# Performance work log

Measured on AMD Instinct MI355X. Metric: run time of the kernel, lower is better.

Reference implementation:

```python
import jax, jax.numpy as jnp
import numpy as np

TEMPERATURE = 0.07
BASE_TEMPERATURE = 0.07


def setup_inputs() -> dict:
    key = jax.random.key(0)
    k1, k2, k3, k4 = jax.random.split(key, 4)
    b, N, d = 1024, 32768, 128
    output_q = jax.random.normal(k1, (b, d), dtype=jnp.float32)
    output_q = output_q / jnp.linalg.norm(output_q, axis=1, keepdims=True)
    queue_all = jax.random.normal(k2, (b + N, d), dtype=jnp.float32)
    queue_all = queue_all / jnp.linalg.norm(queue_all, axis=1, keepdims=True)
    # class flags in [-1, 20); -1 means 'invalid / ignore' per the module's special-casing
    flags = jax.random.randint(k3, (b, 1), -1, 20, dtype=jnp.int32)
    queue_flags_all = jax.random.randint(k4, (b + N, 1), -1, 20, dtype=jnp.int32)
    return {
        "output_q": output_q,
        "queue_all": queue_all,
        "flags": flags,
        "queue_flags_all": queue_flags_all,
        "n_iter": 100,
    }


def reference(output_q, queue_all, flags, queue_flags_all, n_iter):
    b = output_q.shape[0]
    queue = queue_all[b:]            # [N, d]
    qflags = queue_flags_all[b:]     # [N, 1]
    # anchor-vs-queue logits, max-subtracted for stability (max is detached)
    logits = (output_q @ queue.T) / TEMPERATURE                       # [b, N]
    logits = logits - jax.lax.stop_gradient(jnp.max(logits, axis=1, keepdims=True))
    # positive mask: same flag; rows with flag == -1 are fully zeroed
    row_m1 = flags[:, 0] == -1                                        # [b]
    mask_pos = (flags == qflags.T) & (~row_m1[:, None])               # [b, N]
    logits = jnp.where(row_m1[:, None], 0.0, logits)
    lfp = logits * mask_pos                                           # logits_filtered_pos
    if n_iter >= 0:
        # per-row flag revision: if far more entries below the row mean than above,
        # the row's pseudo-label is deemed wrong -> flag := 0, positives zeroed
        mean_sim = lfp.mean(axis=1, keepdims=True)                    # [b, 1]
        pos_cnt = jnp.sum(lfp >= mean_sim, axis=1).astype(jnp.float32)
        wrong_cnt = jnp.sum(lfp < mean_sim, axis=1).astype(jnp.float32)
        revise = (wrong_cnt / (pos_cnt + 1e-6)) > 10.0                # [b]
        flags = jnp.where(revise[:, None], 0, flags)
        lfp = jnp.where(revise[:, None], 0.0, lfp)
    # zero out queue columns whose flag is -1
    col_m1 = qflags[:, 0] == -1                                       # [N]
    logits = jnp.where(col_m1[None, :], 0.0, logits)
    exp_logits = jnp.exp(logits)
    # exact-zero logits (masked entries AND the natural row max) give exp == 1 -> drop them
    exp_logits = exp_logits * (exp_logits != 1.0)
    row_sum = exp_logits.sum(axis=1, keepdims=True)                   # [b, 1]
    log_prob = lfp - jnp.log(row_sum + 1e-12)                         # [b, N]
    num_nonzero = jnp.sum(lfp != 0.0).astype(jnp.float32)             # global count (scalar)
    row_lp = log_prob.sum(axis=1)                                     # [b]
    cond = (num_nonzero > 0) & (row_sum[:, 0] > 0) & (row_lp < 0)     # per-row gate
    loss = jnp.sum(jnp.where(cond, row_lp / num_nonzero, 0.0)) / b
    loss = -(TEMPERATURE / BASE_TEMPERATURE) * loss
    return loss.reshape(1), flags
```

## Files before the change

### kernel.cpp

```cpp
#include <hip/hip_runtime.h>
#include <stdint.h>


typedef short bf16x8 __attribute__((ext_vector_type(8)));
typedef unsigned short ushort8v __attribute__((ext_vector_type(8)));
typedef float f32x4 __attribute__((ext_vector_type(4)));

#define INV_T 14.285714285714286f
#define K2E 20.609929155698604f

__device__ __forceinline__ unsigned short f2bf(float x) {
    unsigned u = __float_as_uint(x);
    return (unsigned short)((u + 0x7FFFu + ((u >> 16) & 1u)) >> 16);
}
__device__ __forceinline__ ushort8v cvt8(const float4* s4) {
    float4 a = s4[0], b = s4[1];
    ushort8v v;
    v[0] = f2bf(a.x); v[1] = f2bf(a.y); v[2] = f2bf(a.z); v[3] = f2bf(a.w);
    v[4] = f2bf(b.x); v[5] = f2bf(b.y); v[6] = f2bf(b.z); v[7] = f2bf(b.w);
    return v;
}
__device__ __forceinline__ void gload_lds16(const void* g, void* l) {
    __builtin_amdgcn_global_load_lds(
        (const __attribute__((address_space(1))) unsigned int*)g,
        (__attribute__((address_space(3))) unsigned int*)l, 16, 0, 0);
}

__global__ void convert_kernel(const float* __restrict__ Q,
                               const float* __restrict__ Kv,
                               const int* __restrict__ qf,
                               unsigned short* __restrict__ Qb,
                               char* __restrict__ KbB,
                               unsigned* __restrict__ histP,
                               unsigned* __restrict__ wrongA, int N, int b) {
    __shared__ unsigned lh[32];
    const int t = threadIdx.x;
    const int blk = blockIdx.x;
    if (blk < 64) {
        if (t < 32) lh[t] = 0u;
        __syncthreads();
        int j0 = blk * 512;
        atomicAdd(&lh[qf[j0 + t] + 1], 1u);
        atomicAdd(&lh[qf[j0 + 256 + t] + 1], 1u);
        __syncthreads();
        if (t < 32) histP[blk * 32 + t] = lh[t];
    }
    int i = blk * 256 + t;
    if (i < b) wrongA[i] = 0u;
    int nk = N * 16;
    if (i < nk) {
        int row = i >> 4, kc = i & 15;
        ushort8v v = cvt8(reinterpret_cast<const float4*>(
            Kv + (size_t)row * 128 + kc * 8));
        int tb = row >> 6, rr = row & 63;
        int off = tb * 16384 + ((rr * 256 + kc * 16) ^ ((rr & 7) << 4));
        *reinterpret_cast<ushort8v*>(KbB + off) = v;
    } else if (i < nk + b * 16) {
        int j = i - nk;
        int row = j >> 4, kc = j & 15;
        ushort8v v = cvt8(reinterpret_cast<const float4*>(
            Q + (size_t)row * 128 + kc * 8));
        *reinterpret_cast<ushort8v*>((char*)Qb + row * 256 + kc * 16) = v;
    }
}

__global__ __launch_bounds__(512, 2) void gemm_kernel(
    const unsigned short* __restrict__ Qb, const char* __restrict__ KbB,
    const int* __restrict__ flags, const int* __restrict__ qf,
    float4* __restrict__ part, int b)
{
    __shared__ __align__(16) char sB[2][16384];
    const int tid = threadIdx.x;
    const int lane = tid & 63, g = lane >> 4, q = lane & 15;
    const int wave = tid >> 6, wr = wave >> 1, wc = wave & 1;
    const int bx = blockIdx.x;
    const int r0 = blockIdx.y * 128;

    bf16x8 af[2][4];
#pragma unroll
    for (int mi = 0; mi < 2; ++mi) {
        int row = r0 + 32 * wr + 16 * mi + q;
#pragma unroll
        for (int ks = 0; ks < 4; ++ks)
            af[mi][ks] = *reinterpret_cast<const bf16x8*>(
                Qb + (size_t)row * 128 + ks * 32 + g * 8);
    }
    unsigned flpack[2];
#pragma unroll
    for (int mi = 0; mi < 2; ++mi) {
        unsigned p = 0;
#pragma unroll
        for (int reg = 0; reg < 4; ++reg) {
            int f = flags[r0 + 32 * wr + 16 * mi + 4 * g + reg];
            unsigned byte = (f < 0) ? 255u : (unsigned)(f + 1);
            p |= byte << (8 * reg);
        }
        flpack[mi] = p;
    }

    float bestp[8], se[8], sl[8];
#pragma unroll
    for (int r = 0; r < 8; ++r) { bestp[r] = -3.0e38f; se[r] = 0.f; sl[r] = 0.f; }

#define STAGE(buf, gt)                                                 \
    {                                                                  \
        const char* s_ = KbB + (size_t)(gt) * 16384 + tid * 16;        \
        char* d_ = &sB[buf][tid * 16];                                 \
        gload_lds16(s_, d_);                                           \
        gload_lds16(s_ + 8192, d_ + 8192);                             \
    }

    STAGE(0, bx * 8);

    for (int t = 0; t < 8; ++t) {
        __syncthreads();
        if (t < 7) STAGE((t + 1) & 1, bx * 8 + t + 1);
        const char* bb = sB[t & 1];

        f32x4 acc[2][2];
#pragma unroll
        for (int mi = 0; mi < 2; ++mi)
#pragma unroll
            for (int ni = 0; ni < 2; ++ni) acc[mi][ni] = (f32x4){0, 0, 0, 0};

#pragma unroll
        for (int ks = 0; ks < 4; ++ks) {
            bf16x8 bf[2];
#pragma unroll
            for (int ni = 0; ni < 2; ++ni) {
                int rr = 32 * wc + 16 * ni + q;
                bf[ni] = *reinterpret_cast<const bf16x8*>(
                    bb + ((rr * 256 + ks * 64 + g * 16) ^ ((rr & 7) << 4)));
            }
#pragma unroll
            for (int mi = 0; mi < 2; ++mi)
#pragma unroll
                for (int ni = 0; ni < 2; ++ni)
                    acc[mi][ni] = __builtin_amdgcn_mfma_f32_16x16x32_bf16(
                        af[mi][ks], bf[ni], acc[mi][ni], 0, 0, 0);
        }

        int cb = bx * 512 + t * 64 + 32 * wc + q;
        unsigned qv1[2] = {(unsigned)(qf[cb] + 1), (unsigned)(qf[cb + 16] + 1)};
#pragma unroll
        for (int mi = 0; mi < 2; ++mi)
#pragma unroll
            for (int reg = 0; reg < 4; ++reg) {
                int rr8 = mi * 4 + reg;
                unsigned fc = (flpack[mi] >> (8 * reg)) & 255u;
                float bp = bestp[rr8], s = se[rr8], l = sl[rr8];
#pragma unroll
                for (int ni = 0; ni < 2; ++ni) {
                    float dot = acc[mi][ni][reg];
                    float e = exp2f(dot * K2E);
                    s += (qv1[ni] == 0u) ? 0.f : e;
                    l += (qv1[ni] == fc) ? dot : 0.f;
                    float dp = __uint_as_float(
                        (__float_as_uint(dot) & ~31u) | qv1[ni]);
                    bp = fmaxf(bp, dp);
                }
                bestp[rr8] = bp; se[rr8] = s; sl[rr8] = l;
            }
    }

    float4* scr = (float4*)sB;
#pragma unroll
    for (int rr8 = 0; rr8 < 8; ++rr8) {
        float bp = bestp[rr8], s = se[rr8], l = sl[rr8];
#pragma unroll
        for (int off = 1; off < 16; off <<= 1) {
            float ob = __shfl_xor(bp, off);
            float os = __shfl_xor(s, off);
            float ol = __shfl_xor(l, off);
            bp = fmaxf(bp, ob);
            s += os;
            l += ol;
        }
        if (q == 0) {
            int rl = 32 * wr + 16 * (rr8 >> 2) + 4 * g + (rr8 & 3);
            scr[wc * 128 + rl] = make_float4(bp, s, l, 0.f);
        }
    }
    __syncthreads();
    if (tid < 128) {
        float4 a = scr[tid], c = scr[128 + tid];
        part[(size_t)bx * b + r0 + tid] =
            make_float4(fmaxf(a.x, c.x), a.y + c.y, a.z + c.z, 0.f);
    }
}

__global__ __launch_bounds__(256) void reduce_kernel(
    const float4* __restrict__ part, const int* __restrict__ flags,
    const unsigned* __restrict__ histP, float* __restrict__ bestA,
    int* __restrict__ flagsA, float* __restrict__ sumlA,
    float* __restrict__ sumexpA, unsigned* __restrict__ cntA, int b)
{
    __shared__ float4 red[4][64];
    __shared__ unsigned sh[32];
    const int t = threadIdx.x;
    if (t < 32) {
        unsigned s = 0;
#pragma unroll
        for (int i = 0; i < 64; ++i) s += histP[i * 32 + t];
        sh[t] = s;
    }
    const int rl = t & 63;
    const int r = blockIdx.x * 64 + rl;
    const int pg = t >> 6;
    float bp = -3.0e38f, s = 0.f, l = 0.f;
    for (int cs = pg; cs < 64; cs += 4) {
        float4 p = part[(size_t)cs * b + r];
        bp = fmaxf(bp, p.x);
        s += p.y;
        l += p.z;
    }
    red[pg][rl] = make_float4(bp, s, l, 0.f);
    __syncthreads();
    if (t < 64) {
        const int rr = blockIdx.x * 64 + t;
        bp = -3.0e38f; s = 0.f; l = 0.f;
#pragma unroll
        for (int i = 0; i < 4; ++i) {
            float4 p = red[i][t];
            bp = fmaxf(bp, p.x);
            s += p.y;
            l += p.z;
        }
        bestA[rr] = bp;
        flagsA[rr] = (int)(__float_as_uint(bp) & 31u);
        sumexpA[rr] = s;
        sumlA[rr] = l;
        int f = flags[rr];
        cntA[rr] = (f >= 0) ? sh[f + 1] : 0u;
    }
}

__global__ void fallback_kernel(const float* __restrict__ Q,
                                const float* __restrict__ Kv,
                                const int* __restrict__ flags,
                                const int* __restrict__ qf,
                                const float* __restrict__ bestA,
                                const float* __restrict__ sumlA,
                                const unsigned* __restrict__ cntA,
                                unsigned* __restrict__ wrongA, int N)
{
    const int r = blockIdx.x;
    unsigned c = cntA[r];
    float ub = (float)c / ((float)(N - (int)c) + 1e-6f);
    if (!(ub > 10.0f)) return;

    __shared__ float sQ[128];
    const int tid = threadIdx.x;
    if (tid < 128) sQ[tid] = Q[(size_t)r * 128 + tid];
    __syncthreads();

    float m = bestA[r] * INV_T;
    float mean = (INV_T * sumlA[r] - (float)c * m) / (float)N;
    int f = flags[r];
    int wp = 0;
    for (int j = tid; j < N; j += 256) {
        float dot = 0.f;
        const float* kr = Kv + (size_t)j * 128;
        for (int k = 0; k < 128; ++k) dot += sQ[k] * kr[k];
        bool mask = (f == qf[j]) && (f != -1);
        float lfp = mask ? (dot * INV_T - m) : 0.f;
        if (lfp < mean) wp++;
    }
    atomicAdd(&wrongA[r], (unsigned)wp);
}

__global__ void final_kernel(const int* __restrict__ flags,
                             const int* __restrict__ n_iter_p,
                             const float* __restrict__ bestA,
                             const int* __restrict__ flagsA,
                             const float* __restrict__ sumlA,
                             const float* __restrict__ sumexpA,
                             const unsigned* __restrict__ cntA,
                             const unsigned* __restrict__ wrongA,
                             float* __restrict__ out, int N, int b)
{
    __shared__ float redf[1024];
    __shared__ unsigned redu[1024];
    const int r = threadIdx.x;

    int f = flags[r];
    bool row_m1 = (f == -1);
    float mdot = bestA[r];
    float m = mdot * INV_T;
    int qmax1 = flagsA[r];
    float s = sumexpA[r];
    float l = sumlA[r];
    unsigned cnt = cntA[r];

    float rowsum;
    if (row_m1) {
        rowsum = 0.f;
    } else {
        float adj = s - ((qmax1 == 0) ? 0.f : exp2f(mdot * K2E));
        rowsum = exp2f(-mdot * K2E) * adj;
        rowsum = fmaxf(rowsum, 0.f);
    }
    float sum_lfp = INV_T * l - (float)cnt * m;
    bool ispos = (!row_m1) && (qmax1 - 1 == f);
    unsigned nnz = cnt - (ispos ? 1u : 0u);

    int nit = *n_iter_p;
    bool revise = false;
    if (nit >= 0) {
        float ub = (float)cnt / ((float)(N - (int)cnt) + 1e-6f);
        if (ub > 10.0f) {
            unsigned wr = wrongA[r];
            float wf = (float)wr;
            float pf = (float)(N - (int)wr);
            revise = (wf / (pf + 1e-6f)) > 10.0f;
        }
    }
    out[1 + r] = (float)(revise ? 0 : f);
    float eff_suml = revise ? 0.f : sum_lfp;
    unsigned eff_nnz = revise ? 0u : nnz;

    redu[r] = eff_nnz;
    __syncthreads();
    for (int ss = 512; ss > 0; ss >>= 1) {
        if (r < ss) redu[r] += redu[r + ss];
        __syncthreads();
    }
    unsigned total_nnz = redu[0];
    __syncthreads();

    float row_lp = eff_suml - (float)N * logf(rowsum + 1e-12f);
    float contrib = (total_nnz > 0u && rowsum > 0.f && row_lp < 0.f)
                        ? row_lp / (float)total_nnz
                        : 0.f;
    redf[r] = contrib;
    __syncthreads();
    for (int ss = 512; ss > 0; ss >>= 1) {
        if (r < ss) redf[r] += redf[r + ss];
        __syncthreads();
    }
    if (r == 0) out[0] = -(redf[0] / (float)b);
}

extern "C" void kernel_launch(void* const* d_in, const int* in_sizes, int n_in,
                              void* d_out, int out_size, void* d_ws,
                              size_t ws_size, hipStream_t stream)
{
    const float* Q = (const float*)d_in[0];
    const float* Kall = (const float*)d_in[1];
    const int* flags = (const int*)d_in[2];
    const int* qfall = (const int*)d_in[3];
    const int* n_iter = (const int*)d_in[4];
    float* out = (float*)d_out;

    const int b = in_sizes[2];
    const int total = in_sizes[3];
    const int N = total - b;
    const float* Kv = Kall + (size_t)b * 128;
    const int* qf = qfall + b;

    char* wsb = (char*)d_ws;
    float* bestA = (float*)wsb;
    int* flagsA = (int*)(wsb + 4096);
    float* sumlA = (float*)(wsb + 8192);
    float* sumexpA = (float*)(wsb + 12288);
    unsigned* cntA = (unsigned*)(wsb + 16384);
    unsigned* wrongA = (unsigned*)(wsb + 20480);
    unsigned* histP = (unsigned*)(wsb + 24576);
    float4* part = (float4*)(wsb + 32768);
    char* KbB = wsb + 32768 + (size_t)64 * b * 16;
    unsigned short* Qb = (unsigned short*)(KbB + (size_t)N * 256);

    int nconv = (N + b) * 16;
    convert_kernel<<<(nconv + 255) / 256, 256, 0, stream>>>(
        Q, Kv, qf, Qb, KbB, histP, wrongA, N, b);

    dim3 grid(N / 512, b / 128);
    gemm_kernel<<<grid, 512, 0, stream>>>(Qb, KbB, flags, qf, part, b);
    reduce_kernel<<<b / 64, 256, 0, stream>>>(part, flags, histP, bestA,
                                              flagsA, sumlA, sumexpA, cntA, b);
    fallback_kernel<<<b, 256, 0, stream>>>(Q, Kv, flags, qf, bestA, sumlA,
                                           cntA, wrongA, N);
    final_kernel<<<1, b, 0, stream>>>(flags, n_iter, bestA, flagsA, sumlA,
                                      sumexpA, cntA, wrongA, out, N, b);
}
```

Measured before the change: 46.81 us.

## Fuse fallback into reduce kernel, fold mask into exp bias, use shuffle reductions

Drops the separate fallback kernel launch. The rare per-row recount of wrong entries now runs inside reduce_kernel, over a block-local list of qualifying rows. In the GEMM epilogue the masked-column select around exp2 is replaced by an FMA with a -1024 bias, so masked columns contribute about zero. final_kernel's shared-memory tree reductions become wavefront shuffle reductions. This saves one launch and several barriers. In exchange, any fallback work is serialized inside a 64-row block, and masked columns now add a tiny nonzero exp term instead of an exact zero.

```diff
diff --git a/kernel.cpp b/kernel.cpp
--- a/kernel.cpp
+++ b/kernel.cpp
@@ -142,6 +142,8 @@
 
         int cb = bx * 512 + t * 64 + 32 * wc + q;
         unsigned qv1[2] = {(unsigned)(qf[cb] + 1), (unsigned)(qf[cb + 16] + 1)};
+        float bias[2] = {(qv1[0] == 0u) ? -1024.f : 0.f,
+                         (qv1[1] == 0u) ? -1024.f : 0.f};
 #pragma unroll
         for (int mi = 0; mi < 2; ++mi)
 #pragma unroll
@@ -152,8 +154,7 @@
 #pragma unroll
                 for (int ni = 0; ni < 2; ++ni) {
                     float dot = acc[mi][ni][reg];
-                    float e = exp2f(dot * K2E);
-                    s += (qv1[ni] == 0u) ? 0.f : e;
+                    s += exp2f(__builtin_fmaf(dot, K2E, bias[ni]));
                     l += (qv1[ni] == fc) ? dot : 0.f;
                     float dp = __uint_as_float(
                         (__float_as_uint(dot) & ~31u) | qv1[ni]);
@@ -191,13 +192,23 @@
 
 __global__ __launch_bounds__(256) void reduce_kernel(
     const float4* __restrict__ part, const int* __restrict__ flags,
-    const unsigned* __restrict__ histP, float* __restrict__ bestA,
-    int* __restrict__ flagsA, float* __restrict__ sumlA,
-    float* __restrict__ sumexpA, unsigned* __restrict__ cntA, int b)
+    const unsigned* __restrict__ histP, const float* __restrict__ Q,
+    const float* __restrict__ Kv, const int* __restrict__ qf,
+    float* __restrict__ bestA, int* __restrict__ flagsA,
+    float* __restrict__ sumlA, float* __restrict__ sumexpA,
+    unsigned* __restrict__ cntA, unsigned* __restrict__ wrongA, int N, int b)
 {
     __shared__ float4 red[4][64];
     __shared__ unsigned sh[32];
+    __shared__ float sB64[64], sL64[64];
+    __shared__ unsigned sC64[64];
+    __shared__ int sList[64];
+    __shared__ int sNum;
+    __shared__ unsigned sWp;
+    __shared__ float sQrow[128];
+
     const int t = threadIdx.x;
+    if (t == 0) sNum = 0;
     if (t < 32) {
         unsigned s = 0;
 #pragma unroll
@@ -231,57 +242,55 @@
         sumexpA[rr] = s;
         sumlA[rr] = l;
         int f = flags[rr];
-        cntA[rr] = (f >= 0) ? sh[f + 1] : 0u;
-    }
-}
-
-__global__ void fallback_kernel(const float* __restrict__ Q,
-                                const float* __restrict__ Kv,
-                                const int* __restrict__ flags,
-                                const int* __restrict__ qf,
-                                const float* __restrict__ bestA,
-                                const float* __restrict__ sumlA,
-                                const unsigned* __restrict__ cntA,
-                                unsigned* __restrict__ wrongA, int N)
+        unsigned c = (f >= 0) ? sh[f + 1] : 0u;
+        cntA[rr] = c;
+        sB64[t] = bp; sL64[t] = l; sC64[t] = c;
+        float ub = (float)c / ((float)(N - (int)c) + 1e-6f);
+        if (ub > 10.0f) {
+            int slot = atomicAdd(&sNum, 1);
+            sList[slot] = t;
+        }
+    }
+    __syncthreads();
+    const int nt = sNum;
+    for (int i = 0; i < nt; ++i) {
+        int rloc = sList[i];
+        int rr = blockIdx.x * 64 + rloc;
+        if (t == 0) sWp = 0u;
+        if (t < 128) sQrow[t] = Q[(size_t)rr * 128 + t];
+        __syncthreads();
+        float m = sB64[rloc] * INV_T;
+        unsigned c = sC64[rloc];
+        float mean = (INV_T * sL64[rloc] - (float)c * m) / (float)N;
+        int f = flags[rr];
+        int wp = 0;
+        for (int j = t; j < N; j += 256) {
+            float dot = 0.f;
+            const float* kr = Kv + (size_t)j * 128;
+            for (int k = 0; k < 128; ++k) dot += sQrow[k] * kr[k];
+            bool mask = (f == qf[j]) && (f != -1);
+            float lfp = mask ? (dot * INV_T - m) : 0.f;
+            if (lfp < mean) wp++;
+        }
+        atomicAdd(&sWp, (unsigned)wp);
+        __syncthreads();
+        if (t == 0) wrongA[rr] = sWp;
+        __syncthreads();
+    }
+}
+
+__global__ __launch_bounds__(1024) void final_kernel(
+    const int* __restrict__ flags, const int* __restrict__ n_iter_p,
+    const float* __restrict__ bestA, const int* __restrict__ flagsA,
+    const float* __restrict__ sumlA, const float* __restrict__ sumexpA,
+    const unsigned* __restrict__ cntA, const unsigned* __restrict__ wrongA,
+    float* __restrict__ out, int N, int b)
 {
-    const int r = blockIdx.x;
-    unsigned c = cntA[r];
-    float ub = (float)c / ((float)(N - (int)c) + 1e-6f);
-    if (!(ub > 10.0f)) return;
-
-    __shared__ float sQ[128];
-    const int tid = threadIdx.x;
-    if (tid < 128) sQ[tid] = Q[(size_t)r * 128 + tid];
-    __syncthreads();
-
-    float m = bestA[r] * INV_T;
-    float mean = (INV_T * sumlA[r] - (float)c * m) / (float)N;
-    int f = flags[r];
-    int wp = 0;
-    for (int j = tid; j < N; j += 256) {
-        float dot = 0.f;
-        const float* kr = Kv + (size_t)j * 128;
-        for (int k = 0; k < 128; ++k) dot += sQ[k] * kr[k];
-        bool mask = (f == qf[j]) && (f != -1);
-        float lfp = mask ? (dot * INV_T - m) : 0.f;
-        if (lfp < mean) wp++;
-    }
-    atomicAdd(&wrongA[r], (unsigned)wp);
-}
-
-__global__ void final_kernel(const int* __restrict__ flags,
-                             const int* __restrict__ n_iter_p,
-                             const float* __restrict__ bestA,
-                             const int* __restrict__ flagsA,
-                             const float* __restrict__ sumlA,
-                             const float* __restrict__ sumexpA,
-                             const unsigned* __restrict__ cntA,
-                             const unsigned* __restrict__ wrongA,
-                             float* __restrict__ out, int N, int b)
-{
-    __shared__ float redf[1024];
-    __shared__ unsigned redu[1024];
+    __shared__ unsigned swU[16];
+    __shared__ float swF[16];
+    __shared__ unsigned sTot;
     const int r = threadIdx.x;
+    const int lane = r & 63, wv = r >> 6;
 
     int f = flags[r];
     bool row_m1 = (f == -1);
@@ -319,26 +328,34 @@
     float eff_suml = revise ? 0.f : sum_lfp;
     unsigned eff_nnz = revise ? 0u : nnz;
 
-    redu[r] = eff_nnz;
-    __syncthreads();
-    for (int ss = 512; ss > 0; ss >>= 1) {
-        if (r < ss) redu[r] += redu[r + ss];
-        __syncthreads();
-    }
-    unsigned total_nnz = redu[0];
-    __syncthreads();
+    unsigned nn = eff_nnz;
+#pragma unroll
+    for (int off = 1; off < 64; off <<= 1) nn += __shfl_xor(nn, off);
+    if (lane == 0) swU[wv] = nn;
+    __syncthreads();
+    if (r == 0) {
+        unsigned tot = 0;
+#pragma unroll
+        for (int i = 0; i < 16; ++i) tot += swU[i];
+        sTot = tot;
+    }
+    __syncthreads();
+    unsigned total_nnz = sTot;
 
     float row_lp = eff_suml - (float)N * logf(rowsum + 1e-12f);
     float contrib = (total_nnz > 0u && rowsum > 0.f && row_lp < 0.f)
                         ? row_lp / (float)total_nnz
                         : 0.f;
-    redf[r] = contrib;
-    __syncthreads();
-    for (int ss = 512; ss > 0; ss >>= 1) {
-        if (r < ss) redf[r] += redf[r + ss];
-        __syncthreads();
-    }
-    if (r == 0) out[0] = -(redf[0] / (float)b);
+#pragma unroll
+    for (int off = 1; off < 64; off <<= 1) contrib += __shfl_xor(contrib, off);
+    if (lane == 0) swF[wv] = contrib;
+    __syncthreads();
+    if (r == 0) {
+        float tot = 0.f;
+#pragma unroll
+        for (int i = 0; i < 16; ++i) tot += swF[i];
+        out[0] = -(tot / (float)b);
+    }
 }
 
 extern "C" void kernel_launch(void* const* d_in, const int* in_sizes, int n_in,
@@ -376,10 +393,9 @@
 
     dim3 grid(N / 512, b / 128);
     gemm_kernel<<<grid, 512, 0, stream>>>(Qb, KbB, flags, qf, part, b);
-    reduce_kernel<<<b / 64, 256, 0, stream>>>(part, flags, histP, bestA,
-                                              flagsA, sumlA, sumexpA, cntA, b);
-    fallback_kernel<<<b, 256, 0, stream>>>(Q, Kv, flags, qf, bestA, sumlA,
-                                           cntA, wrongA, N);
+    reduce_kernel<<<b / 64, 256, 0, stream>>>(part, flags, histP, Q, Kv, qf,
+                                              bestA, flagsA, sumlA, sumexpA,
+                                              cntA, wrongA, N, b);
     final_kernel<<<1, b, 0, stream>>>(flags, n_iter, bestA, flagsA, sumlA,
                                       sumexpA, cntA, wrongA, out, N, b);
 }
```

Measured after the change: 44.17 us (median of 2 runs). -5.6%, faster.
